# Performance work log

Hardware: AMD Instinct MI355X
Metric: run time of the kernel (lower is better)

The kernel has to match this reference:

```python
import jax, jax.numpy as jnp
import numpy as np

B, CIN, COUT, K, NS, NIN, H = 4, 128, 128, 9, 16384, 16384, 64
W0 = 30.0  # SIREN first-layer frequency


def setup_inputs() -> dict:
    ks = jax.random.split(jax.random.key(0), 8)
    x = jax.random.normal(ks[0], (B, CIN, NIN), dtype=jnp.float32)
    neighbours = jax.random.randint(ks[1], (K, NS), 0, NIN)
    # normalized relative neighbour coordinates in [-1, 1], shape (K*NS, 2)
    coords = 2.0 * jax.random.uniform(ks[2], (K * NS, 2), dtype=jnp.float32) - 1.0
    W1 = jax.random.normal(ks[3], (2, H), dtype=jnp.float32) / jnp.sqrt(2.0)
    b1 = jnp.zeros((H,), dtype=jnp.float32)
    W2 = jax.random.normal(ks[4], (H, H), dtype=jnp.float32) / jnp.sqrt(H * 1.0)
    b2 = jnp.zeros((H,), dtype=jnp.float32)
    W3 = jax.random.normal(ks[5], (H, COUT * CIN), dtype=jnp.float32) / jnp.sqrt(H * 1.0)
    b3 = jnp.zeros((COUT * CIN,), dtype=jnp.float32)
    bias = jnp.zeros((1, COUT, 1), dtype=jnp.float32)
    return {"x": x, "neighbours": neighbours, "coords": coords,
            "W1": W1, "b1": b1, "W2": W2, "b2": b2, "W3": W3, "b3": b3,
            "bias": bias}


def reference(x, neighbours, coords, W1, b1, W2, b2, W3, b3, bias):
    k, ns = neighbours.shape
    cin = x.shape[1]
    cout = W3.shape[1] // cin
    # INR filter generation: (K*NS, 2) -> (K*NS, COUT*CIN)
    h = jnp.sin(W0 * (coords @ W1 + b1))
    h = jnp.sin(h @ W2 + b2)
    f = h @ W3 + b3                                  # (K*NS, COUT*CIN)
    # (K*NS, COUT, CIN) -> (COUT, CIN, K, NS), matching torch permute(1,2,0).reshape
    f = f.reshape(k * ns, cout, cin).transpose(1, 2, 0).reshape(cout, cin, k, ns)
    # neighbor gather: (B, CIN, K, NS)
    x_unfold = x[:, :, neighbours]
    # weighted reduce over (CIN, K) per output location
    out = jnp.einsum('bjkl,ijkl->bil', x_unfold, f)
    return out + bias
```

## Files before the change

### kernel.cpp

```cpp
#include <hip/hip_runtime.h>
#include <hip/hip_fp16.h>

#define NS   16384
#define NIN  16384
#define CIN  128
#define COUT 128
#define KNB  9
#define MCH  66
#define QDIM (CIN*MCH)
#define W0C  30.0f

typedef __bf16 bf16;
typedef bf16  bf16x8  __attribute__((ext_vector_type(8)));
typedef _Float16 f16;
typedef unsigned short u16;
typedef u16   u16x8   __attribute__((ext_vector_type(8)));
typedef float floatx4 __attribute__((ext_vector_type(4)));
typedef unsigned int u32;

__device__ inline u16 f2bf(float f){
  u32 u = __float_as_uint(f);
  u += 0x7fffu + ((u >> 16) & 1u);
  return (u16)(u >> 16);
}
__device__ inline float bf2f(u16 s){
  return __uint_as_float((u32)s << 16);
}
__device__ inline u16 f2h(float f){
  f16 h = (f16)f; return __builtin_bit_cast(u16, h);
}
__device__ inline u32 cvtpk2(float lo, float hi){
  u32 r; asm("v_cvt_pk_bf16_f32 %0, %1, %2" : "=v"(r) : "v"(lo), "v"(hi)); return r;
}

#define F2X(f)  f2h(f)
#define X_ONE   0x3C00u

#define WG_BARRIER() do { \
  asm volatile("s_waitcnt lgkmcnt(0)" ::: "memory"); \
  __builtin_amdgcn_s_barrier(); \
} while (0)

#define PREP_K1H  (NS/32)
#define PREP_KTR  2048
#define PREP_K0   ((COUT*QDIM + 1023)/1024)
__global__ __launch_bounds__(1024) void k_prep(
      const float* __restrict__ coords,
      const float* __restrict__ W1, const float* __restrict__ b1,
      const float* __restrict__ W2, const float* __restrict__ b2,
      const float* __restrict__ x,
      const float* __restrict__ W3, const float* __restrict__ b3,
      u32* __restrict__ hK, u16* __restrict__ xT, u16* __restrict__ Vt){
  __shared__ u16 sh[KNB][32][66];
  __shared__ __align__(16) float tfl[4][32][33];
  const int bid = blockIdx.x;
  const int tid = threadIdx.x;

  if (bid < PREP_K1H){
    const int lane = tid & 63;
    const int w    = tid >> 6;
    const int l0   = bid*32;
    for (int e = w; e < KNB*32; e += 16){
      int k = e >> 5, l = e & 31;
      int pt = (k << 14) + l0 + l;
      float c0 = coords[2*pt], c1 = coords[2*pt+1];
      float z  = fmaf(c0, W1[lane], fmaf(c1, W1[64+lane], b1[lane]));
      float h1 = sinf(W0C * z);
      float acc = b2[lane];
      #pragma unroll
      for (int mp = 0; mp < 64; ++mp)
        acc = fmaf(__shfl(h1, mp, 64), W2[mp*64 + lane], acc);
      sh[k][l][lane] = F2X(sinf(acc));
      if (lane == 0){ sh[k][l][64] = X_ONE; sh[k][l][65] = 0; }
    }
    __syncthreads();
    for (int e = tid; e < 66*5*32; e += 1024){
      int m  = e / 160;
      int r  = e - m*160;
      int kp = r >> 5;
      int l  = r & 31;
      u32 lo = sh[2*kp][l][m];
      u32 hi = (kp < 4) ? (u32)sh[2*kp+1][l][m] : 0u;
      hK[(((size_t)m*5 + kp) << 14) + l0 + l] = lo | (hi << 16);
    }
  } else if (bid < PREP_K1H + PREP_KTR){
    const int sub = tid >> 8;
    const int tx  = tid & 31;
    const int ty  = (tid >> 5) & 7;
    const int t   = (bid - PREP_K1H)*4 + sub;
    const int p0  = (t & 511) * 32;
    const int j0  = ((t >> 9) & 3) * 32;
    const int b   = t >> 11;
    const float* xb  = x  + (size_t)b*CIN*NIN;
    u16*         xTb = xT + (size_t)b*NIN*CIN;
    #pragma unroll
    for (int n = 0; n < 4; ++n)
      tfl[sub][ty+8*n][tx] = xb[(size_t)(j0+ty+8*n)*NIN + p0+tx];
    __syncthreads();
    #pragma unroll
    for (int n = 0; n < 4; ++n)
      xTb[(size_t)(p0+ty+8*n)*CIN + j0+tx] = F2X(tfl[sub][tx][ty+8*n]);
  } else {
    int idx = (bid - PREP_K1H - PREP_KTR)*1024 + tid;
    if (idx < COUT*QDIM){
      int i = idx / QDIM;
      int q = idx - i*QDIM;
      int m = q >> 7;
      int j = q & 127;
      float v = 0.f;
      if (m < 64)       v = W3[m*16384 + i*128 + j];
      else if (m == 64) v = b3[i*128 + j];
      Vt[idx] = f2bf(v);
    }
  }
}

__global__ __launch_bounds__(512, 4) void k_fused(
      const u16* __restrict__ xT,
      const u32* __restrict__ hK,
      const int* __restrict__ nb,
      const u16* __restrict__ Vt,
      const float* __restrict__ bias,
      float* __restrict__ out){
  __shared__ __align__(16) u16 A[2][2][32][136];
  __shared__ u32 hs[2][2][5][32];
  __shared__ int pk[KNB][32];

  const int tid = threadIdx.x;
  const int r0  = blockIdx.x * 32;
  const int b   = r0 >> 14;
  const int l0  = r0 & (NS-1);

  if (tid < KNB*32){
    int k = tid >> 5, l = tid & 31;
    pk[k][l] = nb[k*NS + l0 + l];
  }
  WG_BARRIER();

  const int lq = tid >> 4;
  const int jc = tid & 15;

  const bool hact = tid < 320;
  const int  hs_  = tid / 160;
  const int  hr_  = tid - hs_*160;
  const int  hkp_ = hr_ >> 5;
  const int  hl_  = hr_ & 31;
  const u32* hKp  = hK + (((size_t)(5*hs_ + hkp_)) << 14) + l0 + hl_;
  const size_t HSTR = (size_t)10 << 14;
  u32 hra = 0, hrb = 0;
  if (hact){
    u32 h0 = hKp[0];
    hra = hKp[HSTR];
    hrb = hKp[2*HSTR];
    hs[0][hs_][hkp_][hl_] = h0;
  }

  const char* xbB = (const char*)(xT + ((size_t)b << 21));
  u32 xp[5][8];
  #pragma unroll
  for (int kp = 0; kp < 4; ++kp){
    u16x8 ga = *(const u16x8*)(xbB + (((size_t)(u32)pk[2*kp  ][lq]) << 8) + (size_t)jc*16);
    u16x8 gb = *(const u16x8*)(xbB + (((size_t)(u32)pk[2*kp+1][lq]) << 8) + (size_t)jc*16);
    #pragma unroll
    for (int j = 0; j < 8; ++j) xp[kp][j] = (u32)ga[j] | ((u32)gb[j] << 16);
  }
  {
    u16x8 ga = *(const u16x8*)(xbB + (((size_t)(u32)pk[8][lq]) << 8) + (size_t)jc*16);
    #pragma unroll
    for (int j = 0; j < 8; ++j) xp[4][j] = (u32)ga[j];
  }

  const int lane  = tid & 63;
  const int w     = tid >> 6;
  const int iq    = w & 3;
  const int kh    = w >> 2;
  const int ar    = lane & 15;
  const int klane = lane >> 4;

  floatx4 acc[2][2];
  #pragma unroll
  for (int r = 0; r < 2; ++r)
    #pragma unroll
    for (int f = 0; f < 2; ++f)
      acc[r][f] = (floatx4){0.f,0.f,0.f,0.f};

  const char* VtB0 = (const char*)Vt + (size_t)(iq*32      + ar)*(QDIM*2) + (size_t)(kh*128 + klane*16);
  const char* VtB1 = (const char*)Vt + (size_t)(iq*32 + 16 + ar)*(QDIM*2) + (size_t)(kh*128 + klane*16);

  bf16x8 bv[2][4];
  #pragma unroll
  for (int mm = 0; mm < 2; ++mm)
    #pragma unroll
    for (int kt = 0; kt < 2; ++kt){
      bv[0][mm*2+kt] = *(const bf16x8*)(VtB0 + mm*256 + kt*64);
      bv[1][mm*2+kt] = *(const bf16x8*)(VtB1 + mm*256 + kt*64);
    }

  WG_BARRIER();

  for (int mg = 0; mg < 33; ++mg){
    const int pb = mg & 1;

    __half2 ac2[2][8];
    #pragma unroll
    for (int s = 0; s < 2; ++s)
      #pragma unroll
      for (int j = 0; j < 8; ++j) ac2[s][j] = __builtin_bit_cast(__half2, 0u);
    #pragma unroll
    for (int s = 0; s < 2; ++s){
      #pragma unroll
      for (int kp = 0; kp < 5; ++kp){
        __half2 hp = __builtin_bit_cast(__half2, hs[pb][s][kp][lq]);
        #pragma unroll
        for (int j = 0; j < 8; ++j)
          ac2[s][j] = __hfma2(__builtin_bit_cast(__half2, xp[kp][j]), hp, ac2[s][j]);
      }
    }
    {
      float a2[2][8];
      #pragma unroll
      for (int s = 0; s < 2; ++s)
        #pragma unroll
        for (int j = 0; j < 8; ++j)
          a2[s][j] = __low2float(ac2[s][j]) + __high2float(ac2[s][j]);
      uint4 q0, q1;
      q0.x = cvtpk2(a2[0][0], a2[0][1]); q0.y = cvtpk2(a2[0][2], a2[0][3]);
      q0.z = cvtpk2(a2[0][4], a2[0][5]); q0.w = cvtpk2(a2[0][6], a2[0][7]);
      q1.x = cvtpk2(a2[1][0], a2[1][1]); q1.y = cvtpk2(a2[1][2], a2[1][3]);
      q1.z = cvtpk2(a2[1][4], a2[1][5]); q1.w = cvtpk2(a2[1][6], a2[1][7]);
      *(uint4*)&A[pb][0][lq][jc*8] = q0;
      *(uint4*)&A[pb][1][lq][jc*8] = q1;
    }

    if (hact){
      if (mg < 32) hs[pb^1][hs_][hkp_][hl_] = hra;
      hra = hrb;
      if (mg <= 29) hrb = hKp[(size_t)(mg+3)*HSTR];
    }

    WG_BARRIER();

    #pragma unroll
    for (int mm = 0; mm < 2; ++mm){
      const char* Ab = (const char*)&A[pb][mm][0][0] + kh*128 + klane*16;
      #pragma unroll
      for (int kt = 0; kt < 2; ++kt){
        bf16x8 av0 = *(const bf16x8*)(Ab + (     ar)*272 + kt*64);
        bf16x8 av1 = *(const bf16x8*)(Ab + (16 + ar)*272 + kt*64);
        acc[0][0] = __builtin_amdgcn_mfma_f32_16x16x32_bf16(av0, bv[0][mm*2+kt], acc[0][0], 0, 0, 0);
        acc[0][1] = __builtin_amdgcn_mfma_f32_16x16x32_bf16(av0, bv[1][mm*2+kt], acc[0][1], 0, 0, 0);
        acc[1][0] = __builtin_amdgcn_mfma_f32_16x16x32_bf16(av1, bv[0][mm*2+kt], acc[1][0], 0, 0, 0);
        acc[1][1] = __builtin_amdgcn_mfma_f32_16x16x32_bf16(av1, bv[1][mm*2+kt], acc[1][1], 0, 0, 0);
      }
    }

    if (mg < 32){
      const char* Vg0 = VtB0 + (size_t)(mg+1)*512;
      const char* Vg1 = VtB1 + (size_t)(mg+1)*512;
      #pragma unroll
      for (int mm = 0; mm < 2; ++mm)
        #pragma unroll
        for (int kt = 0; kt < 2; ++kt){
          bv[0][mm*2+kt] = *(const bf16x8*)(Vg0 + mm*256 + kt*64);
          bv[1][mm*2+kt] = *(const bf16x8*)(Vg1 + mm*256 + kt*64);
        }
    }
  }

  WG_BARRIER();
  floatx4* red = (floatx4*)&A[0][0][0][0];
  if (kh == 1){
    floatx4* dst = red + (((size_t)iq*64 + lane) << 2);
    dst[0] = acc[0][0]; dst[1] = acc[0][1]; dst[2] = acc[1][0]; dst[3] = acc[1][1];
  }
  WG_BARRIER();
  if (kh == 0){
    const floatx4* src = red + (((size_t)iq*64 + lane) << 2);
    acc[0][0] += src[0]; acc[0][1] += src[1];
    acc[1][0] += src[2]; acc[1][1] += src[3];
    float* ob = out + ((size_t)b << 21);
    #pragma unroll
    for (int rf = 0; rf < 2; ++rf){
      #pragma unroll
      for (int f = 0; f < 2; ++f){
        int i = iq*32 + f*16 + ar;
        float bi = bias[i];
        int l = l0 + rf*16 + klane*4;
        float4 v;
        v.x = acc[rf][f][0] + bi;
        v.y = acc[rf][f][1] + bi;
        v.z = acc[rf][f][2] + bi;
        v.w = acc[rf][f][3] + bi;
        *(float4*)(ob + ((size_t)i << 14) + l) = v;
      }
    }
  }
}

__global__ __launch_bounds__(256) void k_naive(const float* __restrict__ x,
      const int* __restrict__ nb, const float* __restrict__ coords,
      const float* __restrict__ W1, const float* __restrict__ b1,
      const float* __restrict__ W2, const float* __restrict__ b2,
      const float* __restrict__ W3, const float* __restrict__ b3,
      const float* __restrict__ bias, float* __restrict__ out){
  __shared__ __align__(16) float hk[KNB][68];
  __shared__ int pk[KNB];
  __shared__ __align__(16) float xg[4][KNB][128];
  __shared__ __align__(16) float ul[128][66];
  int tid = threadIdx.x;
  int l = blockIdx.x;
  int lane = tid & 63, wid = tid >> 6;
  if (tid < KNB) pk[tid] = nb[tid*NS + l];
  for (int k = wid; k < KNB; k += 4){
    int pt = k*NS + l;
    float c0 = coords[2*pt], c1 = coords[2*pt+1];
    float z  = fmaf(c0, W1[lane], fmaf(c1, W1[64+lane], b1[lane]));
    float h1 = sinf(W0C*z);
    float a = b2[lane];
    for (int mp = 0; mp < 64; ++mp)
      a = fmaf(__shfl(h1, mp, 64), W2[mp*64+lane], a);
    hk[k][lane] = sinf(a);
    if (lane == 0){ hk[k][64] = 1.f; hk[k][65] = 0.f; }
  }
  __syncthreads();
  for (int idx = tid; idx < 4*KNB*128; idx += 256){
    int b = idx / (KNB*128);
    int r = idx - b*KNB*128;
    int k = r >> 7;
    int j = r & 127;
    xg[b][k][j] = x[((size_t)b*CIN + j)*NIN + pk[k]];
  }
  __syncthreads();
  for (int b = 0; b < 4; ++b){
    for (int idx = tid; idx < 128*65; idx += 256){
      int j = idx / 65, m = idx - j*65;
      float s = 0.f;
      for (int k = 0; k < KNB; ++k) s = fmaf(xg[b][k][j], hk[k][m], s);
      ul[j][m] = s;
    }
    __syncthreads();
    if (tid < 128){
      int i = tid;
      float v = bias[i];
      for (int j = 0; j < 128; ++j){
        const float* wcol = W3 + i*128 + j;
        for (int m = 0; m < 64; ++m)
          v = fmaf(ul[j][m], wcol[(size_t)m*16384], v);
        v = fmaf(ul[j][64], b3[i*128+j], v);
      }
      out[((size_t)b<<21) + ((size_t)i<<14) + l] = v;
    }
    __syncthreads();
  }
}

extern "C" void kernel_launch(void* const* d_in, const int* in_sizes, int n_in,
                              void* d_out, int out_size, void* d_ws, size_t ws_size,
                              hipStream_t stream) {
  const float* x      = (const float*)d_in[0];
  const int*   nb     = (const int*)  d_in[1];
  const float* coords = (const float*)d_in[2];
  const float* W1     = (const float*)d_in[3];
  const float* b1     = (const float*)d_in[4];
  const float* W2     = (const float*)d_in[5];
  const float* b2     = (const float*)d_in[6];
  const float* W3     = (const float*)d_in[7];
  const float* b3     = (const float*)d_in[8];
  const float* bias   = (const float*)d_in[9];
  float* out = (float*)d_out;

  const size_t VT_BYTES = (size_t)COUT*QDIM*2;
  const size_t HK_BYTES = (size_t)MCH*5*NS*4;
  const size_t XT_BYTES = (size_t)4*NIN*CIN*2;
  const size_t FIXED    = VT_BYTES + HK_BYTES + XT_BYTES;

  if (ws_size >= FIXED) {
    char* ws = (char*)d_ws;
    unsigned short* Vt = (unsigned short*)ws;
    u32*            hK = (u32*)(ws + VT_BYTES);
    unsigned short* xT = (unsigned short*)(ws + VT_BYTES + HK_BYTES);

    k_prep<<<PREP_K1H + PREP_KTR + PREP_K0, 1024, 0, stream>>>(
        coords, W1, b1, W2, b2, x, W3, b3, hK, xT, Vt);
    k_fused<<<(4*NS)/32, 512, 0, stream>>>(xT, hK, nb, Vt, bias, out);
  } else {
    k_naive<<<NS, 256, 0, stream>>>(x, nb, coords, W1, b1, W2, b2, W3, b3, bias, out);
  }
  (void)in_sizes; (void)n_in; (void)out_size;
}
```

Baseline: 682.8 us.

## Feed MFMA A-operands straight from registers and split waves over K-slices

Each thread's neighbour-weighted x accumulation is now laid out so its bf16 result is already an MFMA A fragment. This removes the per-iteration LDS write and read of the A tile. Each wave now covers all 128 output channels for one quarter of the K dimension and streams Vt B fragments from global memory with a four-deep register prefetch. The four wave partial sums are reduced through shared memory at the end. The cost is more global Vt traffic per wave and eight accumulator tiles per thread. The final prefetch also reads slightly past the last channel block.

```diff
diff --git a/kernel.cpp b/kernel.cpp
--- a/kernel.cpp
+++ b/kernel.cpp
@@ -122,9 +122,9 @@
       const u16* __restrict__ Vt,
       const float* __restrict__ bias,
       float* __restrict__ out){
-  __shared__ __align__(16) u16 A[2][2][32][136];
   __shared__ u32 hs[2][2][5][32];
   __shared__ int pk[KNB][32];
+  __shared__ __align__(16) float redv[3][2][16][128];
 
   const int tid = threadIdx.x;
   const int r0  = blockIdx.x * 32;
@@ -137,8 +137,14 @@
   }
   WG_BARRIER();
 
-  const int lq = tid >> 4;
-  const int jc = tid & 15;
+  const int lane  = tid & 63;
+  const int w     = tid >> 6;
+  const int rf    = w >> 2;
+  const int kt    = w & 3;
+  const int ar    = lane & 15;
+  const int klane = lane >> 4;
+  const int lqp   = rf*16 + ar;
+  const int jcp   = kt*4 + klane;
 
   const bool hact = tid < 320;
   const int  hs_  = tid / 160;
@@ -159,42 +165,27 @@
   u32 xp[5][8];
   #pragma unroll
   for (int kp = 0; kp < 4; ++kp){
-    u16x8 ga = *(const u16x8*)(xbB + (((size_t)(u32)pk[2*kp  ][lq]) << 8) + (size_t)jc*16);
-    u16x8 gb = *(const u16x8*)(xbB + (((size_t)(u32)pk[2*kp+1][lq]) << 8) + (size_t)jc*16);
+    u16x8 ga = *(const u16x8*)(xbB + (((size_t)(u32)pk[2*kp  ][lqp]) << 8) + (size_t)jcp*16);
+    u16x8 gb = *(const u16x8*)(xbB + (((size_t)(u32)pk[2*kp+1][lqp]) << 8) + (size_t)jcp*16);
     #pragma unroll
     for (int j = 0; j < 8; ++j) xp[kp][j] = (u32)ga[j] | ((u32)gb[j] << 16);
   }
   {
-    u16x8 ga = *(const u16x8*)(xbB + (((size_t)(u32)pk[8][lq]) << 8) + (size_t)jc*16);
+    u16x8 ga = *(const u16x8*)(xbB + (((size_t)(u32)pk[8][lqp]) << 8) + (size_t)jcp*16);
     #pragma unroll
     for (int j = 0; j < 8; ++j) xp[4][j] = (u32)ga[j];
   }
 
-  const int lane  = tid & 63;
-  const int w     = tid >> 6;
-  const int iq    = w & 3;
-  const int kh    = w >> 2;
-  const int ar    = lane & 15;
-  const int klane = lane >> 4;
-
-  floatx4 acc[2][2];
+  floatx4 acc[8];
   #pragma unroll
-  for (int r = 0; r < 2; ++r)
-    #pragma unroll
-    for (int f = 0; f < 2; ++f)
-      acc[r][f] = (floatx4){0.f,0.f,0.f,0.f};
-
-  const char* VtB0 = (const char*)Vt + (size_t)(iq*32      + ar)*(QDIM*2) + (size_t)(kh*128 + klane*16);
-  const char* VtB1 = (const char*)Vt + (size_t)(iq*32 + 16 + ar)*(QDIM*2) + (size_t)(kh*128 + klane*16);
-
-  bf16x8 bv[2][4];
+  for (int cf = 0; cf < 8; ++cf) acc[cf] = (floatx4){0.f,0.f,0.f,0.f};
+
+  const char*  baseK = (const char*)Vt + (size_t)ar*(QDIM*2) + kt*64 + klane*16;
+  const size_t CFS   = (size_t)16*QDIM*2;
+  bf16x8 bvw[4];
   #pragma unroll
-  for (int mm = 0; mm < 2; ++mm)
-    #pragma unroll
-    for (int kt = 0; kt < 2; ++kt){
-      bv[0][mm*2+kt] = *(const bf16x8*)(VtB0 + mm*256 + kt*64);
-      bv[1][mm*2+kt] = *(const bf16x8*)(VtB1 + mm*256 + kt*64);
-    }
+  for (int t = 0; t < 4; ++t)
+    bvw[t] = *(const bf16x8*)(baseK + (size_t)(t & 7)*CFS + (size_t)((t>>3))*256);
 
   WG_BARRIER();
 
@@ -210,26 +201,35 @@
     for (int s = 0; s < 2; ++s){
       #pragma unroll
       for (int kp = 0; kp < 5; ++kp){
-        __half2 hp = __builtin_bit_cast(__half2, hs[pb][s][kp][lq]);
+        __half2 hp = __builtin_bit_cast(__half2, hs[pb][s][kp][lqp]);
         #pragma unroll
         for (int j = 0; j < 8; ++j)
           ac2[s][j] = __hfma2(__builtin_bit_cast(__half2, xp[kp][j]), hp, ac2[s][j]);
       }
     }
-    {
-      float a2[2][8];
-      #pragma unroll
-      for (int s = 0; s < 2; ++s)
-        #pragma unroll
-        for (int j = 0; j < 8; ++j)
-          a2[s][j] = __low2float(ac2[s][j]) + __high2float(ac2[s][j]);
-      uint4 q0, q1;
-      q0.x = cvtpk2(a2[0][0], a2[0][1]); q0.y = cvtpk2(a2[0][2], a2[0][3]);
-      q0.z = cvtpk2(a2[0][4], a2[0][5]); q0.w = cvtpk2(a2[0][6], a2[0][7]);
-      q1.x = cvtpk2(a2[1][0], a2[1][1]); q1.y = cvtpk2(a2[1][2], a2[1][3]);
-      q1.z = cvtpk2(a2[1][4], a2[1][5]); q1.w = cvtpk2(a2[1][6], a2[1][7]);
-      *(uint4*)&A[pb][0][lq][jc*8] = q0;
-      *(uint4*)&A[pb][1][lq][jc*8] = q1;
+    bf16x8 frag[2];
+    #pragma unroll
+    for (int s = 0; s < 2; ++s){
+      float a2[8];
+      #pragma unroll
+      for (int j = 0; j < 8; ++j)
+        a2[j] = __low2float(ac2[s][j]) + __high2float(ac2[s][j]);
+      uint4 q;
+      q.x = cvtpk2(a2[0], a2[1]); q.y = cvtpk2(a2[2], a2[3]);
+      q.z = cvtpk2(a2[4], a2[5]); q.w = cvtpk2(a2[6], a2[7]);
+      frag[s] = __builtin_bit_cast(bf16x8, q);
+    }
+
+    #pragma unroll
+    for (int t = 0; t < 16; ++t){
+      const int s  = t >> 3;
+      const int cf = t & 7;
+      acc[cf] = __builtin_amdgcn_mfma_f32_16x16x32_bf16(frag[s], bvw[t & 3], acc[cf], 0, 0, 0);
+      const int u   = t + 4;
+      const int mgu = (u < 16) ? mg : (mg + 1);
+      const int tu  = u & 15;
+      bvw[t & 3] = *(const bf16x8*)(baseK + (size_t)(tu & 7)*CFS
+                                         + (size_t)(mgu*2 + (tu >> 3))*256);
     }
 
     if (hact){
@@ -239,60 +239,35 @@
     }
 
     WG_BARRIER();
-
-    #pragma unroll
-    for (int mm = 0; mm < 2; ++mm){
-      const char* Ab = (const char*)&A[pb][mm][0][0] + kh*128 + klane*16;
-      #pragma unroll
-      for (int kt = 0; kt < 2; ++kt){
-        bf16x8 av0 = *(const bf16x8*)(Ab + (     ar)*272 + kt*64);
-        bf16x8 av1 = *(const bf16x8*)(Ab + (16 + ar)*272 + kt*64);
-        acc[0][0] = __builtin_amdgcn_mfma_f32_16x16x32_bf16(av0, bv[0][mm*2+kt], acc[0][0], 0, 0, 0);
-        acc[0][1] = __builtin_amdgcn_mfma_f32_16x16x32_bf16(av0, bv[1][mm*2+kt], acc[0][1], 0, 0, 0);
-        acc[1][0] = __builtin_amdgcn_mfma_f32_16x16x32_bf16(av1, bv[0][mm*2+kt], acc[1][0], 0, 0, 0);
-        acc[1][1] = __builtin_amdgcn_mfma_f32_16x16x32_bf16(av1, bv[1][mm*2+kt], acc[1][1], 0, 0, 0);
+  }
+
+  if (kt != 0){
+    float* rp = &redv[kt-1][rf][0][0];
+    #pragma unroll
+    for (int cf = 0; cf < 8; ++cf)
+      #pragma unroll
+      for (int j = 0; j < 4; ++j)
+        rp[(klane*4 + j)*128 + cf*16 + ar] = acc[cf][j];
+  }
+  WG_BARRIER();
+  if (kt == 0){
+    float* ob = out + ((size_t)b << 21);
+    const int lbase = l0 + rf*16 + klane*4;
+    #pragma unroll
+    for (int cf = 0; cf < 8; ++cf){
+      const int i  = cf*16 + ar;
+      const float bi = bias[i];
+      float4 v;
+      #pragma unroll
+      for (int j = 0; j < 4; ++j){
+        const int rr = klane*4 + j;
+        float s = acc[cf][j]
+                + redv[0][rf][rr][cf*16 + ar]
+                + redv[1][rf][rr][cf*16 + ar]
+                + redv[2][rf][rr][cf*16 + ar] + bi;
+        (&v.x)[j] = s;
       }
-    }
-
-    if (mg < 32){
-      const char* Vg0 = VtB0 + (size_t)(mg+1)*512;
-      const char* Vg1 = VtB1 + (size_t)(mg+1)*512;
-      #pragma unroll
-      for (int mm = 0; mm < 2; ++mm)
-        #pragma unroll
-        for (int kt = 0; kt < 2; ++kt){
-          bv[0][mm*2+kt] = *(const bf16x8*)(Vg0 + mm*256 + kt*64);
-          bv[1][mm*2+kt] = *(const bf16x8*)(Vg1 + mm*256 + kt*64);
-        }
-    }
-  }
-
-  WG_BARRIER();
-  floatx4* red = (floatx4*)&A[0][0][0][0];
-  if (kh == 1){
-    floatx4* dst = red + (((size_t)iq*64 + lane) << 2);
-    dst[0] = acc[0][0]; dst[1] = acc[0][1]; dst[2] = acc[1][0]; dst[3] = acc[1][1];
-  }
-  WG_BARRIER();
-  if (kh == 0){
-    const floatx4* src = red + (((size_t)iq*64 + lane) << 2);
-    acc[0][0] += src[0]; acc[0][1] += src[1];
-    acc[1][0] += src[2]; acc[1][1] += src[3];
-    float* ob = out + ((size_t)b << 21);
-    #pragma unroll
-    for (int rf = 0; rf < 2; ++rf){
-      #pragma unroll
-      for (int f = 0; f < 2; ++f){
-        int i = iq*32 + f*16 + ar;
-        float bi = bias[i];
-        int l = l0 + rf*16 + klane*4;
-        float4 v;
-        v.x = acc[rf][f][0] + bi;
-        v.y = acc[rf][f][1] + bi;
-        v.z = acc[rf][f][2] + bi;
-        v.w = acc[rf][f][3] + bi;
-        *(float4*)(ob + ((size_t)i << 14) + l) = v;
-      }
+      *(float4*)(ob + ((size_t)i << 14) + lbase) = v;
     }
   }
 }
```

Measured after the change: 1.182 ms. 1.73x slower.
